# Kernel tuning notes

Hardware: AMD Instinct MI355X
Metric: run time of the kernel (lower is better)

## Reference

```python
import jax, jax.numpy as jnp
import numpy as np

N, E, D_IN, HID, H = 50000, 800000, 128, 64, 2
C = HID  # per-head dim (out_channels)


def _lin_params(key, fan_in, fan_out):
    kw, kb = jax.random.split(key)
    s = 1.0 / np.sqrt(fan_in)
    W = jax.random.uniform(kw, (fan_in, fan_out), jnp.float32, -s, s)
    b = jax.random.uniform(kb, (fan_out,), jnp.float32, -s, s)
    return W, b


def setup_inputs() -> dict:
    key = jax.random.key(0)
    ks = jax.random.split(key, 14)
    x = jax.random.normal(ks[0], (N, D_IN), jnp.float32)
    edge_index = jax.random.randint(ks[1], (2, E), 0, N, jnp.int32)
    inp = {"x": x, "edge_index": edge_index}
    dims = [D_IN, HID, HID]
    i = 2
    for L, d_in in enumerate(dims, start=1):
        for nm, fo in (("q", H * C), ("k", H * C), ("v", H * C), ("s", HID)):
            W, b = _lin_params(ks[i], d_in, fo)
            inp[f"W{L}{nm}"] = W
            inp[f"b{L}{nm}"] = b
            i += 1
            if i >= 14:
                ks = jax.random.split(ks[-1], 14)
                i = 0
    return inp


def _transformer_conv(x, src, dst, Wq, bq, Wk, bk, Wv, bv, Ws, bs):
    # x: [N, d_in] -> out: [N, HID]
    q = (x @ Wq + bq).reshape(N, H, C)
    k = (x @ Wk + bk).reshape(N, H, C)
    v = (x @ Wv + bv).reshape(N, H, C)
    qi = q[dst]                      # [E, H, C] gather at destination (query)
    kj = k[src]                      # [E, H, C] gather at source (key)
    alpha = jnp.sum(qi * kj, axis=-1) / jnp.sqrt(jnp.float32(C))  # [E, H]
    amax = jax.ops.segment_max(alpha, dst, num_segments=N)        # [N, H]
    ex = jnp.exp(alpha - amax[dst])                               # [E, H]
    denom = jax.ops.segment_sum(ex, dst, num_segments=N)          # [N, H]
    attn = ex / (denom[dst] + 1e-16)                              # [E, H]
    msg = v[src] * attn[:, :, None]                               # [E, H, C]
    out = jax.ops.segment_sum(msg, dst, num_segments=N)           # [N, H, C]
    out = out.mean(axis=1)                                        # concat=False: head mean
    return out + x @ Ws + bs                                      # root skip


def reference(x, edge_index,
              W1q, b1q, W1k, b1k, W1v, b1v, W1s, b1s,
              W2q, b2q, W2k, b2k, W2v, b2v, W2s, b2s,
              W3q, b3q, W3k, b3k, W3v, b3v, W3s, b3s):
    src, dst = edge_index[0], edge_index[1]
    h = jax.nn.relu(_transformer_conv(x, src, dst, W1q, b1q, W1k, b1k, W1v, b1v, W1s, b1s))
    h = jax.nn.relu(_transformer_conv(h, src, dst, W2q, b2q, W2k, b2k, W2v, b2v, W2s, b2s))
    h = jax.nn.relu(_transformer_conv(h, src, dst, W3q, b3q, W3k, b3k, W3v, b3v, W3s, b3s))
    return h
```

## Files before the change

kernel.cpp:

```cpp
#include <hip/hip_runtime.h>
#include <cstdint>

typedef _Float16 f16;
typedef __attribute__((ext_vector_type(2))) _Float16 f16x2;
typedef __attribute__((ext_vector_type(8))) _Float16 f16x8;
typedef __attribute__((ext_vector_type(4))) float f32x4;


__global__ void hist_kernel(const int* __restrict__ dst, int* __restrict__ cnt, int E) {
    int e = blockIdx.x * blockDim.x + threadIdx.x;
    if (e < E) atomicAdd(&cnt[dst[e]], 1);
}

__global__ __launch_bounds__(256) void block_scan_kernel(
    const int* __restrict__ cnt, int* __restrict__ rowptr,
    int* __restrict__ partials, int n) {
    __shared__ int lds[256];
    int tid = threadIdx.x;
    int i = blockIdx.x * 256 + tid;
    int v = (i < n) ? cnt[i] : 0;
    lds[tid] = v;
    __syncthreads();
    for (int off = 1; off < 256; off <<= 1) {
        int t = (tid >= off) ? lds[tid - off] : 0;
        __syncthreads();
        lds[tid] += t;
        __syncthreads();
    }
    if (i < n) rowptr[i + 1] = lds[tid];
    if (tid == 255) partials[blockIdx.x] = lds[255];
}

__global__ __launch_bounds__(256) void partial_scan_kernel(int* __restrict__ partials, int nb) {
    __shared__ int lds[256];
    int tid = threadIdx.x;
    int v = (tid < nb) ? partials[tid] : 0;
    lds[tid] = v;
    __syncthreads();
    for (int off = 1; off < 256; off <<= 1) {
        int t = (tid >= off) ? lds[tid - off] : 0;
        __syncthreads();
        lds[tid] += t;
        __syncthreads();
    }
    if (tid < nb) partials[tid] = lds[tid] - v;
}

__global__ __launch_bounds__(256) void add_offsets_kernel(
    int* __restrict__ rowptr, const int* __restrict__ partials, int n) {
    int i = blockIdx.x * 256 + threadIdx.x;
    if (i < n) rowptr[i + 1] += partials[blockIdx.x];
    if (i == 0) rowptr[0] = 0;
}

__global__ void scatter_kernel(const int* __restrict__ src, const int* __restrict__ dst,
                               const int* __restrict__ rowptr, int* __restrict__ cnt,
                               int* __restrict__ src_sorted, int E) {
    int e = blockIdx.x * blockDim.x + threadIdx.x;
    if (e < E) {
        int d = dst[e];
        int p = rowptr[d] + atomicAdd(&cnt[d], 1);
        src_sorted[p] = src[e];
    }
}


__global__ __launch_bounds__(256) void cvt_kernel(const float* __restrict__ in,
                                                  f16* __restrict__ out, int n8) {
    int i = blockIdx.x * 256 + threadIdx.x;
    if (i >= n8) return;
    float4 a = ((const float4*)in)[2 * i];
    float4 b = ((const float4*)in)[2 * i + 1];
    f16x8 o = {(f16)a.x, (f16)a.y, (f16)a.z, (f16)a.w,
               (f16)b.x, (f16)b.y, (f16)b.z, (f16)b.w};
    *(f16x8*)(out + 8 * i) = o;
}


__global__ __launch_bounds__(256) void prep_w_kernel(
    const float* __restrict__ Wq, const float* __restrict__ Wk,
    const float* __restrict__ Wv, const float* __restrict__ Ws,
    const float* __restrict__ bq, const float* __restrict__ bk,
    const float* __restrict__ bv, const float* __restrict__ bs,
    f16* __restrict__ Wt, float* __restrict__ bias, int K) {
    int idx = blockIdx.x * 256 + threadIdx.x;
    if (idx < 448) {
        bias[idx] = (idx < 128) ? bq[idx]
                  : (idx < 256) ? bk[idx - 128]
                  : (idx < 384) ? bv[idx - 256]
                  : bs[idx - 384];
    }
    if (idx >= 448 * K) return;
    int c = idx / K, k = idx - c * K;
    float v;
    if (c < 128)      v = Wq[k * 128 + c];
    else if (c < 256) v = Wk[k * 128 + (c - 128)];
    else if (c < 384) v = Wv[k * 128 + (c - 256)];
    else              v = Ws[k * 64 + (c - 384)];
    Wt[(size_t)c * K + k] = (f16)v;
}


template <int K>
__global__ __launch_bounds__(256) void gemm_qkvs_kernel(
    const f16* __restrict__ X, const f16* __restrict__ Wt,
    const float* __restrict__ bias, f16* __restrict__ out, int M) {
    __shared__ f16 xa[64 * K];
    __shared__ f16 wb[64 * K];
    constexpr int CPR = K / 8;
    int row0 = blockIdx.x * 64, col0 = blockIdx.y * 64;
    int tid = threadIdx.x;

    for (int c = tid; c < 64 * CPR; c += 256) {
        int r = c / CPR, kc = c % CPR;
        int gr = row0 + r;
        uint4 v = {0, 0, 0, 0};
        if (gr < M) v = *(const uint4*)(X + (size_t)gr * K + kc * 8);
        int off = (r * K + kc * 8) * 2;
        off ^= (r & 7) << 4;
        *(uint4*)((char*)xa + off) = v;
    }
    for (int c = tid; c < 64 * CPR; c += 256) {
        int r = c / CPR, kc = c % CPR;
        uint4 v = *(const uint4*)(Wt + (size_t)(col0 + r) * K + kc * 8);
        int off = (r * K + kc * 8) * 2;
        off ^= (r & 7) << 4;
        *(uint4*)((char*)wb + off) = v;
    }
    __syncthreads();

    int lane = tid & 63, wid = tid >> 6;
    int fr = lane & 15, fk = lane >> 4;
    int arow = wid * 16 + fr;
    f32x4 acc[4] = {};

    for (int ks = 0; ks < K; ks += 32) {
        int aoff = (arow * K + ks + fk * 8) * 2;
        aoff ^= (arow & 7) << 4;
        f16x8 af = *(f16x8*)((char*)xa + aoff);
        #pragma unroll
        for (int ct = 0; ct < 4; ++ct) {
            int brow = ct * 16 + fr;
            int boff = (brow * K + ks + fk * 8) * 2;
            boff ^= (brow & 7) << 4;
            f16x8 bf = *(f16x8*)((char*)wb + boff);
            acc[ct] = __builtin_amdgcn_mfma_f32_16x16x32_f16(af, bf, acc[ct], 0, 0, 0);
        }
    }

    int orow = row0 + wid * 16 + fk * 4;
    int ocol = col0 + fr;
    #pragma unroll
    for (int ct = 0; ct < 4; ++ct) {
        float b = bias[ocol + ct * 16];
        #pragma unroll
        for (int r = 0; r < 4; ++r) {
            int gr = orow + r;
            if (gr < M) out[(size_t)gr * 448 + ocol + ct * 16] = (f16)(acc[ct][r] + b);
        }
    }
}


__global__ __launch_bounds__(256) void attn_kernel(
    const f16* __restrict__ T,
    const int* __restrict__ rowptr, const int* __restrict__ srcs,
    f16* __restrict__ hout, float* __restrict__ fout, int n, int final_layer) {
    int node = blockIdx.x * 4 + (threadIdx.x >> 6);
    if (node >= n) return;
    int lane = threadIdx.x & 63;
    int c8 = lane & 7, h = (lane >> 3) & 1, e2 = lane >> 4;
    const size_t base = (size_t)node * 448;
    const int coff = h * 64 + c8 * 8;

    f16x8 q = *(const f16x8*)(T + base + coff);
    float m = -__builtin_inff(), s = 0.f;
    float av[8] = {};

    int beg = rowptr[node], end = rowptr[node + 1];
    for (int i0 = beg; i0 < end; i0 += 4) {
        int i = i0 + e2;
        bool valid = (i < end);
        int sidx = srcs[valid ? i : (end - 1)];
        const f16* p = T + (size_t)sidx * 448 + coff;
        f16x8 kv = *(const f16x8*)(p + 128);
        f16x8 vv = *(const f16x8*)(p + 256);
        float d = 0.f;
        #pragma unroll
        for (int j = 0; j < 8; ++j) d += (float)q[j] * (float)kv[j];
        d += __shfl_xor(d, 1);
        d += __shfl_xor(d, 2);
        d += __shfl_xor(d, 4);
        d *= 0.125f;
        if (!valid) d = -__builtin_inff();
        float dmax = fmaxf(d, __shfl_xor(d, 16));
        dmax = fmaxf(dmax, __shfl_xor(dmax, 32));
        float nm = fmaxf(m, dmax);
        float f  = __expf(m - nm);
        float pe = __expf(d - nm);
        s = s * f + pe;
        #pragma unroll
        for (int j = 0; j < 8; ++j) av[j] = av[j] * f + pe * (float)vv[j];
        m = nm;
    }

    s += __shfl_xor(s, 16);
    s += __shfl_xor(s, 32);
    float inv = 1.0f / (s + 1e-16f);
    float r[8];
    #pragma unroll
    for (int j = 0; j < 8; ++j) {
        float a = av[j];
        a += __shfl_xor(a, 16);
        a += __shfl_xor(a, 32);
        r[j] = a * inv;
    }
    #pragma unroll
    for (int j = 0; j < 8; ++j) r[j] = 0.5f * (r[j] + __shfl_xor(r[j], 8));

    if (lane < 8) {
        f16x8 sk = *(const f16x8*)(T + base + 384 + c8 * 8);
        #pragma unroll
        for (int j = 0; j < 8; ++j) r[j] = fmaxf(r[j] + (float)sk[j], 0.f);
        if (final_layer) {
            float4 o0 = make_float4(r[0], r[1], r[2], r[3]);
            float4 o1 = make_float4(r[4], r[5], r[6], r[7]);
            float4* dst4 = (float4*)(fout + (size_t)node * 64 + c8 * 8);
            dst4[0] = o0;
            dst4[1] = o1;
        } else {
            f16x8 o = {(f16)r[0], (f16)r[1], (f16)r[2], (f16)r[3],
                       (f16)r[4], (f16)r[5], (f16)r[6], (f16)r[7]};
            *(f16x8*)(hout + (size_t)node * 64 + c8 * 8) = o;
        }
    }
}


extern "C" void kernel_launch(void* const* d_in, const int* in_sizes, int n_in,
                              void* d_out, int out_size, void* d_ws, size_t ws_size,
                              hipStream_t stream) {
    const float* x = (const float*)d_in[0];
    const int* ei  = (const int*)d_in[1];
    const int N = in_sizes[0] / 128;
    const int E = in_sizes[1] / 2;
    const int* src = ei;
    const int* dst = ei + E;

    const float* Wq[3] = {(const float*)d_in[2],  (const float*)d_in[10], (const float*)d_in[18]};
    const float* bq[3] = {(const float*)d_in[3],  (const float*)d_in[11], (const float*)d_in[19]};
    const float* Wk[3] = {(const float*)d_in[4],  (const float*)d_in[12], (const float*)d_in[20]};
    const float* bk[3] = {(const float*)d_in[5],  (const float*)d_in[13], (const float*)d_in[21]};
    const float* Wv[3] = {(const float*)d_in[6],  (const float*)d_in[14], (const float*)d_in[22]};
    const float* bv[3] = {(const float*)d_in[7],  (const float*)d_in[15], (const float*)d_in[23]};
    const float* Wsk[3]= {(const float*)d_in[8],  (const float*)d_in[16], (const float*)d_in[24]};
    const float* bsk[3]= {(const float*)d_in[9],  (const float*)d_in[17], (const float*)d_in[25]};

    char* p = (char*)d_ws;
    int* rowptr   = (int*)p; p += (size_t)(N + 1) * 4;
    int* cnt      = (int*)p; p += (size_t)N * 4;
    int* srcs     = (int*)p; p += (size_t)E * 4;
    int* partials = (int*)p; p += 256 * 4;
    p = (char*)(((uintptr_t)p + 255) & ~(uintptr_t)255);
    f16* X16  = (f16*)p; p += (size_t)N * 128 * 2;
    f16* Xh   = (f16*)p; p += (size_t)N * 64 * 2;
    f16* QKVS = (f16*)p; p += (size_t)N * 448 * 2;
    f16* Wt   = (f16*)p; p += (size_t)448 * 128 * 2;
    float* bias = (float*)p; p += 448 * 4;
    if ((size_t)(p - (char*)d_ws) > ws_size) return;

    int nb = (N + 255) / 256;
    hipMemsetAsync(cnt, 0, (size_t)N * 4, stream);
    hist_kernel<<<(E + 255) / 256, 256, 0, stream>>>(dst, cnt, E);
    block_scan_kernel<<<nb, 256, 0, stream>>>(cnt, rowptr, partials, N);
    partial_scan_kernel<<<1, 256, 0, stream>>>(partials, nb);
    add_offsets_kernel<<<nb, 256, 0, stream>>>(rowptr, partials, N);
    hipMemsetAsync(cnt, 0, (size_t)N * 4, stream);
    scatter_kernel<<<(E + 255) / 256, 256, 0, stream>>>(src, dst, rowptr, cnt, srcs, E);

    cvt_kernel<<<(N * 128 / 8 + 255) / 256, 256, 0, stream>>>(x, X16, N * 128 / 8);

    int gx = (N + 63) / 64;
    for (int l = 0; l < 3; ++l) {
        int K = (l == 0) ? 128 : 64;
        prep_w_kernel<<<(448 * K + 255) / 256, 256, 0, stream>>>(
            Wq[l], Wk[l], Wv[l], Wsk[l], bq[l], bk[l], bv[l], bsk[l], Wt, bias, K);
        if (l == 0)
            gemm_qkvs_kernel<128><<<dim3(gx, 7), 256, 0, stream>>>(X16, Wt, bias, QKVS, N);
        else
            gemm_qkvs_kernel<64><<<dim3(gx, 7), 256, 0, stream>>>(Xh, Wt, bias, QKVS, N);
        attn_kernel<<<(N + 3) / 4, 256, 0, stream>>>(
            QKVS, rowptr, srcs, Xh, (float*)d_out, N, (l == 2) ? 1 : 0);
    }
}
```

Baseline: 373.2 us.

## Fuse f32-to-f16 conversion into GEMM, loop columns in-block, lazy softmax rescale

Drops the separate conversion kernel by having the first-layer GEMM read f32 input and convert while staging into LDS. Each GEMM block now loads its A tile once, keeps the fragments in registers, and loops over all 7 column tiles, so the input is no longer re-read for every column tile. The attention kernel uses fdot2 for the q·k dot product and rescales the online-softmax running max only when a score exceeds it by more than a threshold. This cuts exp and rescale work, at the cost of fewer GEMM blocks in flight, extra barriers inside each block, and a bounded-overflow assumption in the softmax.

```diff
diff --git a/kernel.cpp b/kernel.cpp
--- a/kernel.cpp
+++ b/kernel.cpp
@@ -3,8 +3,15 @@
 
 typedef _Float16 f16;
 typedef __attribute__((ext_vector_type(2))) _Float16 f16x2;
+typedef __attribute__((ext_vector_type(4))) _Float16 f16x4;
 typedef __attribute__((ext_vector_type(8))) _Float16 f16x8;
 typedef __attribute__((ext_vector_type(4))) float f32x4;
+
+#if defined(__has_builtin)
+# if __has_builtin(__builtin_amdgcn_fdot2)
+#  define HAVE_FDOT2 1
+# endif
+#endif
 
 
 __global__ void hist_kernel(const int* __restrict__ dst, int* __restrict__ cnt, int E) {
@@ -62,18 +69,6 @@
         int p = rowptr[d] + atomicAdd(&cnt[d], 1);
         src_sorted[p] = src[e];
     }
-}
-
-
-__global__ __launch_bounds__(256) void cvt_kernel(const float* __restrict__ in,
-                                                  f16* __restrict__ out, int n8) {
-    int i = blockIdx.x * 256 + threadIdx.x;
-    if (i >= n8) return;
-    float4 a = ((const float4*)in)[2 * i];
-    float4 b = ((const float4*)in)[2 * i + 1];
-    f16x8 o = {(f16)a.x, (f16)a.y, (f16)a.z, (f16)a.w,
-               (f16)b.x, (f16)b.y, (f16)b.z, (f16)b.w};
-    *(f16x8*)(out + 8 * i) = o;
 }
 
 
@@ -101,62 +96,91 @@
 }
 
 
-template <int K>
+template <int K, bool F32IN>
 __global__ __launch_bounds__(256) void gemm_qkvs_kernel(
-    const f16* __restrict__ X, const f16* __restrict__ Wt,
+    const void* __restrict__ Xv, const f16* __restrict__ Wt,
     const float* __restrict__ bias, f16* __restrict__ out, int M) {
     __shared__ f16 xa[64 * K];
     __shared__ f16 wb[64 * K];
-    constexpr int CPR = K / 8;
-    int row0 = blockIdx.x * 64, col0 = blockIdx.y * 64;
+    int row0 = blockIdx.x * 64;
     int tid = threadIdx.x;
 
-    for (int c = tid; c < 64 * CPR; c += 256) {
-        int r = c / CPR, kc = c % CPR;
-        int gr = row0 + r;
-        uint4 v = {0, 0, 0, 0};
-        if (gr < M) v = *(const uint4*)(X + (size_t)gr * K + kc * 8);
-        int off = (r * K + kc * 8) * 2;
-        off ^= (r & 7) << 4;
-        *(uint4*)((char*)xa + off) = v;
-    }
-    for (int c = tid; c < 64 * CPR; c += 256) {
-        int r = c / CPR, kc = c % CPR;
-        uint4 v = *(const uint4*)(Wt + (size_t)(col0 + r) * K + kc * 8);
-        int off = (r * K + kc * 8) * 2;
-        off ^= (r & 7) << 4;
-        *(uint4*)((char*)wb + off) = v;
+    if (F32IN) {
+        const float* X = (const float*)Xv;
+        constexpr int CPR = K / 4;
+        for (int c = tid; c < 64 * CPR; c += 256) {
+            int r = c / CPR, kc = c % CPR;
+            int gr = row0 + r;
+            float4 v = {0.f, 0.f, 0.f, 0.f};
+            if (gr < M) v = *(const float4*)(X + (size_t)gr * K + kc * 4);
+            f16x4 hv = {(f16)v.x, (f16)v.y, (f16)v.z, (f16)v.w};
+            int off = (r * K + kc * 4) * 2;
+            off ^= (r & 7) << 4;
+            *(f16x4*)((char*)xa + off) = hv;
+        }
+    } else {
+        const f16* X = (const f16*)Xv;
+        constexpr int CPR = K / 8;
+        for (int c = tid; c < 64 * CPR; c += 256) {
+            int r = c / CPR, kc = c % CPR;
+            int gr = row0 + r;
+            uint4 v = {0, 0, 0, 0};
+            if (gr < M) v = *(const uint4*)(X + (size_t)gr * K + kc * 8);
+            int off = (r * K + kc * 8) * 2;
+            off ^= (r & 7) << 4;
+            *(uint4*)((char*)xa + off) = v;
+        }
     }
     __syncthreads();
 
     int lane = tid & 63, wid = tid >> 6;
     int fr = lane & 15, fk = lane >> 4;
     int arow = wid * 16 + fr;
-    f32x4 acc[4] = {};
-
-    for (int ks = 0; ks < K; ks += 32) {
-        int aoff = (arow * K + ks + fk * 8) * 2;
+    constexpr int NK = K / 32;
+    f16x8 af[NK];
+    #pragma unroll
+    for (int ks = 0; ks < NK; ++ks) {
+        int aoff = (arow * K + ks * 32 + fk * 8) * 2;
         aoff ^= (arow & 7) << 4;
-        f16x8 af = *(f16x8*)((char*)xa + aoff);
-        #pragma unroll
-        for (int ct = 0; ct < 4; ++ct) {
-            int brow = ct * 16 + fr;
-            int boff = (brow * K + ks + fk * 8) * 2;
-            boff ^= (brow & 7) << 4;
-            f16x8 bf = *(f16x8*)((char*)wb + boff);
-            acc[ct] = __builtin_amdgcn_mfma_f32_16x16x32_f16(af, bf, acc[ct], 0, 0, 0);
-        }
+        af[ks] = *(f16x8*)((char*)xa + aoff);
     }
 
     int orow = row0 + wid * 16 + fk * 4;
-    int ocol = col0 + fr;
-    #pragma unroll
-    for (int ct = 0; ct < 4; ++ct) {
-        float b = bias[ocol + ct * 16];
-        #pragma unroll
-        for (int r = 0; r < 4; ++r) {
-            int gr = orow + r;
-            if (gr < M) out[(size_t)gr * 448 + ocol + ct * 16] = (f16)(acc[ct][r] + b);
+    constexpr int CPRW = K / 8;
+    for (int ct = 0; ct < 7; ++ct) {
+        if (ct > 0) __syncthreads();
+        int col0 = ct * 64;
+        for (int c = tid; c < 64 * CPRW; c += 256) {
+            int r = c / CPRW, kc = c % CPRW;
+            uint4 v = *(const uint4*)(Wt + (size_t)(col0 + r) * K + kc * 8);
+            int off = (r * K + kc * 8) * 2;
+            off ^= (r & 7) << 4;
+            *(uint4*)((char*)wb + off) = v;
+        }
+        __syncthreads();
+
+        f32x4 acc[4] = {};
+        #pragma unroll
+        for (int ks = 0; ks < NK; ++ks) {
+            #pragma unroll
+            for (int cf = 0; cf < 4; ++cf) {
+                int brow = cf * 16 + fr;
+                int boff = (brow * K + ks * 32 + fk * 8) * 2;
+                boff ^= (brow & 7) << 4;
+                f16x8 bf = *(f16x8*)((char*)wb + boff);
+                acc[cf] = __builtin_amdgcn_mfma_f32_16x16x32_f16(af[ks], bf, acc[cf], 0, 0, 0);
+            }
+        }
+
+        int ocol = col0 + fr;
+        #pragma unroll
+        for (int cf = 0; cf < 4; ++cf) {
+            float b = bias[ocol + cf * 16];
+            #pragma unroll
+            for (int r = 0; r < 4; ++r) {
+                int gr = orow + r;
+                if (gr < M) out[(size_t)gr * 448 + ocol + cf * 16] = (f16)(acc[cf][r] + b);
+            }
         }
     }
 }
@@ -169,9 +193,9 @@
     int node = blockIdx.x * 4 + (threadIdx.x >> 6);
     if (node >= n) return;
     int lane = threadIdx.x & 63;
-    int c8 = lane & 7, h = (lane >> 3) & 1, e2 = lane >> 4;
+    int c8 = lane & 7, e2 = lane >> 4;
     const size_t base = (size_t)node * 448;
-    const int coff = h * 64 + c8 * 8;
+    const int coff = ((lane >> 3) & 1) * 64 + c8 * 8;
 
     f16x8 q = *(const f16x8*)(T + base + coff);
     float m = -__builtin_inff(), s = 0.f;
@@ -186,22 +210,37 @@
         f16x8 kv = *(const f16x8*)(p + 128);
         f16x8 vv = *(const f16x8*)(p + 256);
         float d = 0.f;
+#ifdef HAVE_FDOT2
+        #pragma unroll
+        for (int j = 0; j < 4; ++j) {
+            f16x2 qq = {q[2 * j], q[2 * j + 1]};
+            f16x2 kk = {kv[2 * j], kv[2 * j + 1]};
+            d = __builtin_amdgcn_fdot2(qq, kk, d, false);
+        }
+#else
         #pragma unroll
         for (int j = 0; j < 8; ++j) d += (float)q[j] * (float)kv[j];
+#endif
         d += __shfl_xor(d, 1);
         d += __shfl_xor(d, 2);
         d += __shfl_xor(d, 4);
         d *= 0.125f;
         if (!valid) d = -__builtin_inff();
-        float dmax = fmaxf(d, __shfl_xor(d, 16));
-        dmax = fmaxf(dmax, __shfl_xor(dmax, 32));
-        float nm = fmaxf(m, dmax);
-        float f  = __expf(m - nm);
-        float pe = __expf(d - nm);
-        s = s * f + pe;
-        #pragma unroll
-        for (int j = 0; j < 8; ++j) av[j] = av[j] * f + pe * (float)vv[j];
-        m = nm;
+
+        if (__any(d > m + 6.f)) {
+            float dmax = fmaxf(d, __shfl_xor(d, 16));
+            dmax = fmaxf(dmax, __shfl_xor(dmax, 32));
+            float nm = fmaxf(m, dmax);
+            float f = __expf(m - nm);
+            s *= f;
+            #pragma unroll
+            for (int j = 0; j < 8; ++j) av[j] *= f;
+            m = nm;
+        }
+        float pe = __expf(d - m);
+        s += pe;
+        #pragma unroll
+        for (int j = 0; j < 8; ++j) av[j] += pe * (float)vv[j];
     }
 
     s += __shfl_xor(s, 16);
@@ -223,11 +262,9 @@
         #pragma unroll
         for (int j = 0; j < 8; ++j) r[j] = fmaxf(r[j] + (float)sk[j], 0.f);
         if (final_layer) {
-            float4 o0 = make_float4(r[0], r[1], r[2], r[3]);
-            float4 o1 = make_float4(r[4], r[5], r[6], r[7]);
             float4* dst4 = (float4*)(fout + (size_t)node * 64 + c8 * 8);
-            dst4[0] = o0;
-            dst4[1] = o1;
+            dst4[0] = make_float4(r[0], r[1], r[2], r[3]);
+            dst4[1] = make_float4(r[4], r[5], r[6], r[7]);
         } else {
             f16x8 o = {(f16)r[0], (f16)r[1], (f16)r[2], (f16)r[3],
                        (f16)r[4], (f16)r[5], (f16)r[6], (f16)r[7]};
@@ -262,7 +299,6 @@
     int* srcs     = (int*)p; p += (size_t)E * 4;
     int* partials = (int*)p; p += 256 * 4;
     p = (char*)(((uintptr_t)p + 255) & ~(uintptr_t)255);
-    f16* X16  = (f16*)p; p += (size_t)N * 128 * 2;
     f16* Xh   = (f16*)p; p += (size_t)N * 64 * 2;
     f16* QKVS = (f16*)p; p += (size_t)N * 448 * 2;
     f16* Wt   = (f16*)p; p += (size_t)448 * 128 * 2;
@@ -278,17 +314,15 @@
     hipMemsetAsync(cnt, 0, (size_t)N * 4, stream);
     scatter_kernel<<<(E + 255) / 256, 256, 0, stream>>>(src, dst, rowptr, cnt, srcs, E);
 
-    cvt_kernel<<<(N * 128 / 8 + 255) / 256, 256, 0, stream>>>(x, X16, N * 128 / 8);
-
     int gx = (N + 63) / 64;
     for (int l = 0; l < 3; ++l) {
         int K = (l == 0) ? 128 : 64;
         prep_w_kernel<<<(448 * K + 255) / 256, 256, 0, stream>>>(
             Wq[l], Wk[l], Wv[l], Wsk[l], bq[l], bk[l], bv[l], bsk[l], Wt, bias, K);
         if (l == 0)
-            gemm_qkvs_kernel<128><<<dim3(gx, 7), 256, 0, stream>>>(X16, Wt, bias, QKVS, N);
+            gemm_qkvs_kernel<128, true><<<gx, 256, 0, stream>>>(x, Wt, bias, QKVS, N);
         else
-            gemm_qkvs_kernel<64><<<dim3(gx, 7), 256, 0, stream>>>(Xh, Wt, bias, QKVS, N);
+            gemm_qkvs_kernel<64, false><<<gx, 256, 0, stream>>>(Xh, Wt, bias, QKVS, N);
         attn_kernel<<<(N + 3) / 4, 256, 0, stream>>>(
             QKVS, rowptr, srcs, Xh, (float*)d_out, N, (l == 2) ? 1 : 0);
     }
```

Measured after the change: 373.6 us. Within noise of the previous version (+0.1%).
